# Kernel optimization log

Measured on AMD Instinct MI355X. Metric: run time of the kernel, lower is better.

The kernel has to match this reference:

```python
import jax, jax.numpy as jnp
import numpy as np

EPS = 1e-4  # Moller-Trumbore epsilon from the original

def _dot(a, b):
    return jnp.sum(a * b, axis=-1)

def setup_inputs() -> dict:
    key = jax.random.key(0)
    k1, k2, k3 = jax.random.split(key, 3)
    N, V, F = 2048, 2500, 4096
    p = jax.random.normal(k1, (N, 3), dtype=jnp.float32)
    v = jax.random.normal(k2, (V, 3), dtype=jnp.float32)
    f = jax.random.randint(k3, (F, 3), 0, V, dtype=jnp.int64)
    return {"p": p, "v": v, "f": f}

def reference(p, v, f):
    N = p.shape[0]
    faces = v[f]                      # (F,3,3)
    a, b, c = faces[:, 0], faces[:, 1], faces[:, 2]   # (F,3) each
    pe = p[None]                      # (1,N,3), broadcasts against (F,1,3)

    # --- point-to-triangle distance = min over the 3 edge segments (matches original output math) ---
    e1 = a - b                        # faces[:,0]-faces[:,1]
    e2 = c - b
    e3 = c - a

    def seg(e, ref_pt, q0, q1):
        # s = ((ref_pt - p) . e) / |e|^2, clamped; closest = s*q0 + (1-s)*q1  (original formula kept verbatim)
        m2 = _dot(e, e)[:, None]                       # (F,1)
        s = jnp.clip(_dot(ref_pt[:, None] - pe, e[:, None]) / m2, 0.0, 1.0)[..., None]  # (F,N,1)
        cl = s * q0[:, None] + (1.0 - s) * q1[:, None]  # (F,N,3)
        d = jnp.linalg.norm(cl - pe, axis=-1)           # (F,N)
        return d, cl

    d12, c12 = seg(e1, a, b, a)   # s12 from (p0-p).e1; closest = s*p1+(1-s)*p0
    d23, c23 = seg(e2, c, b, c)   # s23 from (p2-p).e2; closest = s*p1+(1-s)*p2
    d31, c31 = seg(e3, c, a, c)   # s31 from (p2-p).e3; closest = s*p0+(1-s)*p2

    d_all = jnp.stack([d12, d23, d31], axis=0)          # (3,F,N)
    c_all = jnp.stack([c12, c23, c31], axis=0)          # (3,F,N,3)
    which = jnp.argmin(d_all, axis=0)                   # (F,N)
    dist = jnp.min(d_all, axis=0)                       # (F,N)
    closest = jnp.take_along_axis(c_all, which[None, ..., None], axis=0)[0]  # (F,N,3)

    # nearest face per query point
    fidx = jnp.argmin(jnp.abs(dist), axis=0)            # (N,)
    dmin = jnp.take_along_axis(dist, fidx[None], axis=0)  # (1,N)
    closest_p = closest[fidx, jnp.arange(N)]            # (N,3)

    # --- Moller-Trumbore ray-triangle parity test toward mesh centroid ---
    dirv = v.mean(axis=0)[None] - p                     # (N,3)
    me1 = b - a                                         # faces[:,1]-faces[:,0]
    me2 = c - a
    pvec = jnp.cross(dirv[None], me2[:, None])          # (F,N,3)
    det = _dot(me1[:, None], pvec)                      # (F,N)
    tvec = pe - a[:, None]                              # (F,N,3)
    u = _dot(tvec, pvec) / det
    qvec = jnp.cross(tvec, me1[:, None])                # (F,N,3)
    dd = _dot(dirv[None], qvec) / det
    t = _dot(me2[:, None], qvec) / det
    hit = (jnp.abs(det) > EPS) & (u >= 0) & (u <= 1) & (dd >= 0) & (u + dd <= 1) & (t > EPS)
    counts = jnp.sum(hit, axis=0)                       # (N,)
    inside = (0.5 - (counts % 2 == 1).astype(dmin.dtype)) * 2.0  # +1 outside, -1 inside

    dmin = dmin * inside[None]                          # (1,N)
    return (dmin, closest_p)
```

## Files before the change

kernel.cpp:

```cpp
#include <hip/hip_runtime.h>
#include <math.h>

#define TRI_EPS 1e-4f

__global__ __launch_bounds__(256) void prep_kernel(
    const float* __restrict__ v, const int* __restrict__ f,
    float4* __restrict__ fdat6, float4* __restrict__ fdat5,
    float* __restrict__ vm, int V, int F) {
    const int t = threadIdx.x;
    const int j = blockIdx.x * 256 + t;
    if (j < F) {
        const int i0 = f[3 * j + 0];
        const int i1 = f[3 * j + 1];
        const int i2 = f[3 * j + 2];
        const float ax = v[3 * i0 + 0], ay = v[3 * i0 + 1], az = v[3 * i0 + 2];
        const float bx = v[3 * i1 + 0], by = v[3 * i1 + 1], bz = v[3 * i1 + 2];
        const float cx = v[3 * i2 + 0], cy = v[3 * i2 + 1], cz = v[3 * i2 + 2];
        const float e1x = ax - bx, e1y = ay - by, e1z = az - bz;
        const float e2x = cx - bx, e2y = cy - by, e2z = cz - bz;
        const float e3x = cx - ax, e3y = cy - ay, e3z = cz - az;
        const float m1 = e1x * e1x + e1y * e1y + e1z * e1z;
        const float m2 = e2x * e2x + e2y * e2y + e2z * e2z;
        const float m3 = e3x * e3x + e3y * e3y + e3z * e3z;
        const float inv1 = 1.f / m1, inv2 = 1.f / m2, inv3 = 1.f / m3;
        fdat6[6 * j + 0] = make_float4(ax, ay, az, inv1);
        fdat6[6 * j + 1] = make_float4(bx, by, bz, inv2);
        fdat6[6 * j + 2] = make_float4(cx, cy, cz, inv3);
        fdat6[6 * j + 3] = make_float4(e1x, e1y, e1z, 0.f);
        fdat6[6 * j + 4] = make_float4(e2x, e2y, e2z, 0.f);
        fdat6[6 * j + 5] = make_float4(e3x, e3y, e3z, 0.f);
        fdat5[5 * j + 0] = make_float4(ax, ay, az, inv1);
        fdat5[5 * j + 1] = make_float4(cx, cy, cz, inv2);
        fdat5[5 * j + 2] = make_float4(e1x, e1y, e1z, inv3);
        fdat5[5 * j + 3] = make_float4(e2x, e2y, e2z, 0.f);
        fdat5[5 * j + 4] = make_float4(e3x, e3y, e3z, 0.f);
    }
    if (blockIdx.x == 0) {
        __shared__ float sx[256], sy[256], sz[256];
        float x = 0.f, y = 0.f, z = 0.f;
        for (int i = t; i < V; i += 256) {
            x += v[3 * i + 0];
            y += v[3 * i + 1];
            z += v[3 * i + 2];
        }
        sx[t] = x; sy[t] = y; sz[t] = z;
        __syncthreads();
        for (int off = 128; off > 0; off >>= 1) {
            if (t < off) {
                sx[t] += sx[t + off];
                sy[t] += sy[t + off];
                sz[t] += sz[t + off];
            }
            __syncthreads();
        }
        if (t == 0) {
            vm[0] = sx[0] / (float)V;
            vm[1] = sy[0] / (float)V;
            vm[2] = sz[0] / (float)V;
        }
    }
}

struct FP {
    float d1, d2, d3;
    float x1, y1, z1, x2, y2, z2, x3, y3, z3;
    float apx, apy, apz;
};

__device__ __forceinline__ FP face_point(
    const float4 ra, const float4 rb, const float4 rc,
    const float e1x, const float e1y, const float e1z,
    const float e2x, const float e2y, const float e2z,
    const float e3x, const float e3y, const float e3z,
    const float px, const float py, const float pz) {
    FP r;
    const float ax = ra.x, ay = ra.y, az = ra.z;
    const float bx = rb.x, by = rb.y, bz = rb.z;
    const float cx = rc.x, cy = rc.y, cz = rc.z;
    r.apx = ax - px; r.apy = ay - py; r.apz = az - pz;
    const float cpx = cx - px, cpy = cy - py, cpz = cz - pz;

    float s1 = (r.apx * e1x + r.apy * e1y + r.apz * e1z) * ra.w;
    s1 = fminf(fmaxf(s1, 0.f), 1.f);
    const float o1 = 1.f - s1;
    r.x1 = s1 * bx + o1 * ax;
    r.y1 = s1 * by + o1 * ay;
    r.z1 = s1 * bz + o1 * az;
    float ux = r.x1 - px, uy = r.y1 - py, uz = r.z1 - pz;
    r.d1 = ux * ux + uy * uy + uz * uz;

    float s2 = (cpx * e2x + cpy * e2y + cpz * e2z) * rb.w;
    s2 = fminf(fmaxf(s2, 0.f), 1.f);
    const float o2 = 1.f - s2;
    r.x2 = s2 * bx + o2 * cx;
    r.y2 = s2 * by + o2 * cy;
    r.z2 = s2 * bz + o2 * cz;
    ux = r.x2 - px; uy = r.y2 - py; uz = r.z2 - pz;
    r.d2 = ux * ux + uy * uy + uz * uz;

    float s3 = (cpx * e3x + cpy * e3y + cpz * e3z) * rc.w;
    s3 = fminf(fmaxf(s3, 0.f), 1.f);
    const float o3 = 1.f - s3;
    r.x3 = s3 * ax + o3 * cx;
    r.y3 = s3 * ay + o3 * cy;
    r.z3 = s3 * az + o3 * cz;
    ux = r.x3 - px; uy = r.y3 - py; uz = r.z3 - pz;
    r.d3 = ux * ux + uy * uy + uz * uz;
    return r;
}

__device__ __forceinline__ void pair_lean(
    const float4 r0, const float4 r1, const float4 r2,
    const float4 r3, const float4 r4,
    const float px, const float py, const float pz,
    const float dx, const float dy, const float dz, const int j,
    float& bd2, int& bid, int& hits) {
    const float apx = r0.x - px, apy = r0.y - py, apz = r0.z - pz;
    const float cpx = r1.x - px, cpy = r1.y - py, cpz = r1.z - pz;
    const float e1x = r2.x, e1y = r2.y, e1z = r2.z;
    const float e2x = r3.x, e2y = r3.y, e2z = r3.z;
    const float e3x = r4.x, e3y = r4.y, e3z = r4.z;

    float s1 = (apx * e1x + apy * e1y + apz * e1z) * r0.w;
    s1 = fminf(fmaxf(s1, 0.f), 1.f);
    const float u1x = apx - s1 * e1x;
    const float u1y = apy - s1 * e1y;
    const float u1z = apz - s1 * e1z;
    const float d1 = u1x * u1x + u1y * u1y + u1z * u1z;

    float s2 = (cpx * e2x + cpy * e2y + cpz * e2z) * r1.w;
    s2 = fminf(fmaxf(s2, 0.f), 1.f);
    const float u2x = cpx - s2 * e2x;
    const float u2y = cpy - s2 * e2y;
    const float u2z = cpz - s2 * e2z;
    const float d2 = u2x * u2x + u2y * u2y + u2z * u2z;

    float s3 = (cpx * e3x + cpy * e3y + cpz * e3z) * r2.w;
    s3 = fminf(fmaxf(s3, 0.f), 1.f);
    const float u3x = cpx - s3 * e3x;
    const float u3y = cpy - s3 * e3y;
    const float u3z = cpz - s3 * e3z;
    const float d3 = u3x * u3x + u3y * u3y + u3z * u3z;

    float fd2 = d1; int eid = 0;
    if (d2 < fd2) { fd2 = d2; eid = 1; }
    if (d3 < fd2) { fd2 = d3; eid = 2; }
    if (fd2 < bd2) { bd2 = fd2; bid = (j << 2) | eid; }

    const float pvx = dy * e3z - dz * e3y;
    const float pvy = dz * e3x - dx * e3z;
    const float pvz = dx * e3y - dy * e3x;
    const float det = -(e1x * pvx + e1y * pvy + e1z * pvz);
    const float tu = -(apx * pvx + apy * pvy + apz * pvz);
    const float qvx = apy * e1z - apz * e1y;
    const float qvy = apz * e1x - apx * e1z;
    const float qvz = apx * e1y - apy * e1x;
    const float td = dx * qvx + dy * qvy + dz * qvz;
    const float tn = e3x * qvx + e3y * qvy + e3z * qvz;
    const float adet = fabsf(det);
    const float sd = (det > 0.f) ? 1.f : -1.f;
    const float su = tu * sd;
    const float sq = td * sd;
    const float st = tn * sd;
    if (adet > TRI_EPS && su >= 0.f && su <= adet && sq >= 0.f &&
        (su + sq) <= adet && st > TRI_EPS * adet)
        hits++;
}

template <int CS>
__global__ __launch_bounds__(256) void sdf_main_t(
    const float* __restrict__ p, const float4* __restrict__ fd5,
    const float* __restrict__ vm,
    unsigned long long* __restrict__ keysP, unsigned* __restrict__ hitsP,
    int N, int C) {
    __shared__ float4 sfd[5 * CS];
    const int t = threadIdx.x;
    const int k = blockIdx.x % C;
    const int pg = blockIdx.x / C;
    const int j0 = k * CS;

    if (t < 5 * CS) sfd[t] = fd5[5 * j0 + t];

    const int i = pg * 256 + t;
    const bool vld = (i < N);
    const int li = vld ? i : 0;
    const float px = p[3 * li + 0];
    const float py = p[3 * li + 1];
    const float pz = p[3 * li + 2];
    const float dx = vm[0] - px;
    const float dy = vm[1] - py;
    const float dz = vm[2] - pz;

    float bd2 = INFINITY; int bid = 0x7fffffff; int hits = 0;

    __syncthreads();

    #pragma unroll 4
    for (int jj = 0; jj < CS; ++jj) {
        pair_lean(sfd[5 * jj + 0], sfd[5 * jj + 1], sfd[5 * jj + 2],
                  sfd[5 * jj + 3], sfd[5 * jj + 4],
                  px, py, pz, dx, dy, dz, j0 + jj, bd2, bid, hits);
    }

    if (vld) {
        const unsigned long long key =
            ((unsigned long long)__float_as_uint(bd2) << 32) | (unsigned int)bid;
        keysP[(size_t)k * N + i] = key;
        hitsP[(size_t)k * N + i] = (unsigned)hits;
    }
}

__global__ __launch_bounds__(256) void sdf_main_g(
    const float* __restrict__ p, const float4* __restrict__ fd5,
    const float* __restrict__ vm,
    unsigned long long* __restrict__ keysP, unsigned* __restrict__ hitsP,
    int N, int F, int C, int CS) {
    const int k = blockIdx.x % C;
    const int pg = blockIdx.x / C;
    const int i = pg * 256 + threadIdx.x;
    if (i >= N) return;
    const float px = p[3 * i + 0];
    const float py = p[3 * i + 1];
    const float pz = p[3 * i + 2];
    const float dx = vm[0] - px;
    const float dy = vm[1] - py;
    const float dz = vm[2] - pz;
    float bd2 = INFINITY; int bid = 0x7fffffff; int hits = 0;
    const int j0 = k * CS;
    const int j1 = min(F, j0 + CS);
    for (int j = j0; j < j1; ++j) {
        pair_lean(fd5[5 * j + 0], fd5[5 * j + 1], fd5[5 * j + 2],
                  fd5[5 * j + 3], fd5[5 * j + 4],
                  px, py, pz, dx, dy, dz, j, bd2, bid, hits);
    }
    const unsigned long long key =
        ((unsigned long long)__float_as_uint(bd2) << 32) | (unsigned int)bid;
    keysP[(size_t)k * N + i] = key;
    hitsP[(size_t)k * N + i] = (unsigned)hits;
}

__global__ __launch_bounds__(256) void sdf_reduce_epi(
    const float* __restrict__ p, const float4* __restrict__ fd6,
    const unsigned long long* __restrict__ keysP,
    const unsigned* __restrict__ hitsP,
    float* __restrict__ out, int N, int C) {
    const int t = threadIdx.x;
    const int q = t & 63;
    const int w = t >> 6;
    const int i = blockIdx.x * 64 + q;

    unsigned long long bk = 0xFFFFFFFFFFFFFFFFull;
    unsigned hs = 0;
    if (i < N) {
        const int kpw = C >> 2;
        int k = w * kpw;
        #pragma unroll 4
        for (int kk = 0; kk < kpw; ++kk, ++k) {
            const unsigned long long kv = keysP[(size_t)k * N + i];
            if (kv < bk) bk = kv;
            hs += hitsP[(size_t)k * N + i];
        }
    }
    __shared__ unsigned long long sk[4][64];
    __shared__ unsigned sh[4][64];
    sk[w][q] = bk;
    sh[w][q] = hs;
    __syncthreads();
    if (w == 0 && i < N) {
        #pragma unroll
        for (int ww = 1; ww < 4; ++ww) {
            const unsigned long long kv = sk[ww][q];
            if (kv < bk) bk = kv;
            hs += sh[ww][q];
        }
        const float bd2 = __uint_as_float((unsigned int)(bk >> 32));
        const int bid = (int)(unsigned int)(bk & 0xFFFFFFFFull);
        const int jw = bid >> 2;
        const int eid = bid & 3;
        const float px = p[3 * i + 0];
        const float py = p[3 * i + 1];
        const float pz = p[3 * i + 2];
        const float4 wa  = fd6[6 * jw + 0];
        const float4 wb  = fd6[6 * jw + 1];
        const float4 wc  = fd6[6 * jw + 2];
        const float4 we1 = fd6[6 * jw + 3];
        const float4 we2 = fd6[6 * jw + 4];
        const float4 we3 = fd6[6 * jw + 5];
        const FP r = face_point(wa, wb, wc, we1.x, we1.y, we1.z,
                                we2.x, we2.y, we2.z, we3.x, we3.y, we3.z,
                                px, py, pz);
        float clx = r.x1, cly = r.y1, clz = r.z1;
        if (eid == 1) { clx = r.x2; cly = r.y2; clz = r.z2; }
        if (eid == 2) { clx = r.x3; cly = r.y3; clz = r.z3; }
        const float d = sqrtf(bd2);
        out[i] = (hs & 1u) ? -d : d;
        out[N + 3 * i + 0] = clx;
        out[N + 3 * i + 1] = cly;
        out[N + 3 * i + 2] = clz;
    }
}

extern "C" void kernel_launch(void* const* d_in, const int* in_sizes, int n_in,
                              void* d_out, int out_size, void* d_ws,
                              size_t ws_size, hipStream_t stream) {
    const float* p = (const float*)d_in[0];
    const float* v = (const float*)d_in[1];
    const int* f = (const int*)d_in[2];
    float* out = (float*)d_out;

    const int N = in_sizes[0] / 3;
    const int V = in_sizes[1] / 3;
    const int F = in_sizes[2] / 3;

    const int C = 256;

    char* base = (char*)d_ws;
    float* vm = (float*)base;
    unsigned long long* keysP = (unsigned long long*)(base + 16);
    unsigned* hitsP = (unsigned*)(base + 16 + 8ull * C * N);
    size_t off = 16 + 12ull * C * N;
    off = (off + 15) & ~15ull;
    float4* fdat6 = (float4*)(base + off);
    float4* fdat5 = (float4*)(base + off + 6ull * F * sizeof(float4));

    prep_kernel<<<(F + 255) / 256, 256, 0, stream>>>(v, f, fdat6, fdat5, vm,
                                                     V, F);

    const int npg = (N + 255) / 256;
    if (F == C * 16) {
        sdf_main_t<16><<<npg * C, 256, 0, stream>>>(p, fdat5, vm, keysP, hitsP,
                                                    N, C);
    } else {
        const int CS = (F + C - 1) / C;
        sdf_main_g<<<npg * C, 256, 0, stream>>>(p, fdat5, vm, keysP, hitsP,
                                                N, F, C, CS);
    }
    sdf_reduce_epi<<<(N + 63) / 64, 256, 0, stream>>>(p, fdat6, keysP, hitsP,
                                                      out, N, C);
}
```

Before: 44.18 us.

## Process two query points per thread and split faces into more chunks

```diff
diff --git a/kernel.cpp b/kernel.cpp
--- a/kernel.cpp
+++ b/kernel.cpp
@@ -168,7 +168,7 @@
 }
 
 template <int CS>
-__global__ __launch_bounds__(256) void sdf_main_t(
+__global__ __launch_bounds__(256) void sdf_main2_t(
     const float* __restrict__ p, const float4* __restrict__ fd5,
     const float* __restrict__ vm,
     unsigned long long* __restrict__ keysP, unsigned* __restrict__ hitsP,
@@ -181,32 +181,46 @@
 
     if (t < 5 * CS) sfd[t] = fd5[5 * j0 + t];
 
-    const int i = pg * 256 + t;
-    const bool vld = (i < N);
-    const int li = vld ? i : 0;
-    const float px = p[3 * li + 0];
-    const float py = p[3 * li + 1];
-    const float pz = p[3 * li + 2];
-    const float dx = vm[0] - px;
-    const float dy = vm[1] - py;
-    const float dz = vm[2] - pz;
-
-    float bd2 = INFINITY; int bid = 0x7fffffff; int hits = 0;
+    const int iA = pg * 512 + t;
+    const int iB = iA + 256;
+    const bool vA = (iA < N);
+    const bool vB = (iB < N);
+    const int lA = vA ? iA : 0;
+    const int lB = vB ? iB : 0;
+    const float pAx = p[3 * lA + 0], pAy = p[3 * lA + 1], pAz = p[3 * lA + 2];
+    const float pBx = p[3 * lB + 0], pBy = p[3 * lB + 1], pBz = p[3 * lB + 2];
+    const float vmx = vm[0], vmy = vm[1], vmz = vm[2];
+    const float dAx = vmx - pAx, dAy = vmy - pAy, dAz = vmz - pAz;
+    const float dBx = vmx - pBx, dBy = vmy - pBy, dBz = vmz - pBz;
+
+    float Ad2 = INFINITY; int Aid = 0x7fffffff; int Ah = 0;
+    float Bd2 = INFINITY; int Bid = 0x7fffffff; int Bh = 0;
 
     __syncthreads();
 
-    #pragma unroll 4
+    #pragma unroll 2
     for (int jj = 0; jj < CS; ++jj) {
-        pair_lean(sfd[5 * jj + 0], sfd[5 * jj + 1], sfd[5 * jj + 2],
-                  sfd[5 * jj + 3], sfd[5 * jj + 4],
-                  px, py, pz, dx, dy, dz, j0 + jj, bd2, bid, hits);
-    }
-
-    if (vld) {
-        const unsigned long long key =
-            ((unsigned long long)__float_as_uint(bd2) << 32) | (unsigned int)bid;
-        keysP[(size_t)k * N + i] = key;
-        hitsP[(size_t)k * N + i] = (unsigned)hits;
+        const float4 r0 = sfd[5 * jj + 0];
+        const float4 r1 = sfd[5 * jj + 1];
+        const float4 r2 = sfd[5 * jj + 2];
+        const float4 r3 = sfd[5 * jj + 3];
+        const float4 r4 = sfd[5 * jj + 4];
+        const int j = j0 + jj;
+        pair_lean(r0, r1, r2, r3, r4, pAx, pAy, pAz, dAx, dAy, dAz, j,
+                  Ad2, Aid, Ah);
+        pair_lean(r0, r1, r2, r3, r4, pBx, pBy, pBz, dBx, dBy, dBz, j,
+                  Bd2, Bid, Bh);
+    }
+
+    if (vA) {
+        keysP[(size_t)k * N + iA] =
+            ((unsigned long long)__float_as_uint(Ad2) << 32) | (unsigned int)Aid;
+        hitsP[(size_t)k * N + iA] = (unsigned)Ah;
+    }
+    if (vB) {
+        keysP[(size_t)k * N + iB] =
+            ((unsigned long long)__float_as_uint(Bd2) << 32) | (unsigned int)Bid;
+        hitsP[(size_t)k * N + iB] = (unsigned)Bh;
     }
 }
 
@@ -233,9 +247,8 @@
                   fd5[5 * j + 3], fd5[5 * j + 4],
                   px, py, pz, dx, dy, dz, j, bd2, bid, hits);
     }
-    const unsigned long long key =
+    keysP[(size_t)k * N + i] =
         ((unsigned long long)__float_as_uint(bd2) << 32) | (unsigned int)bid;
-    keysP[(size_t)k * N + i] = key;
     hitsP[(size_t)k * N + i] = (unsigned)hits;
 }
 
@@ -312,7 +325,8 @@
     const int V = in_sizes[1] / 3;
     const int F = in_sizes[2] / 3;
 
-    const int C = 256;
+    const int C = 512;
+    const int CS = 8;
 
     char* base = (char*)d_ws;
     float* vm = (float*)base;
@@ -326,14 +340,15 @@
     prep_kernel<<<(F + 255) / 256, 256, 0, stream>>>(v, f, fdat6, fdat5, vm,
                                                      V, F);
 
-    const int npg = (N + 255) / 256;
-    if (F == C * 16) {
-        sdf_main_t<16><<<npg * C, 256, 0, stream>>>(p, fdat5, vm, keysP, hitsP,
-                                                    N, C);
+    if (F == C * CS) {
+        const int npg = (N + 511) / 512;
+        sdf_main2_t<CS><<<npg * C, 256, 0, stream>>>(p, fdat5, vm, keysP,
+                                                     hitsP, N, C);
     } else {
-        const int CS = (F + C - 1) / C;
+        const int CSg = (F + C - 1) / C;
+        const int npg = (N + 255) / 256;
         sdf_main_g<<<npg * C, 256, 0, stream>>>(p, fdat5, vm, keysP, hitsP,
-                                                N, F, C, CS);
+                                                N, F, C, CSg);
     }
     sdf_reduce_epi<<<(N + 63) / 64, 256, 0, stream>>>(p, fdat6, keysP, hitsP,
                                                       out, N, C);
```

After: 53.23 us. +20.5%, slower.

## Transpose main kernel to thread-per-face with swizzle reductions over 16-face groups

Applied to the files above, without the earlier changes.

```diff
diff --git a/kernel.cpp b/kernel.cpp
--- a/kernel.cpp
+++ b/kernel.cpp
@@ -167,46 +167,120 @@
         hits++;
 }
 
-template <int CS>
-__global__ __launch_bounds__(256) void sdf_main_t(
+#define SWZF(x, imm) \
+    __int_as_float(__builtin_amdgcn_ds_swizzle(__float_as_int(x), imm))
+
+template <int PC>
+__global__ __launch_bounds__(256, 8) void sdf_tr(
     const float* __restrict__ p, const float4* __restrict__ fd5,
     const float* __restrict__ vm,
     unsigned long long* __restrict__ keysP, unsigned* __restrict__ hitsP,
-    int N, int C) {
-    __shared__ float4 sfd[5 * CS];
+    int N, int FB) {
     const int t = threadIdx.x;
-    const int k = blockIdx.x % C;
-    const int pg = blockIdx.x / C;
-    const int j0 = k * CS;
-
-    if (t < 5 * CS) sfd[t] = fd5[5 * j0 + t];
-
-    const int i = pg * 256 + t;
-    const bool vld = (i < N);
-    const int li = vld ? i : 0;
-    const float px = p[3 * li + 0];
-    const float py = p[3 * li + 1];
-    const float pz = p[3 * li + 2];
-    const float dx = vm[0] - px;
-    const float dy = vm[1] - py;
-    const float dz = vm[2] - pz;
-
-    float bd2 = INFINITY; int bid = 0x7fffffff; int hits = 0;
-
+    const int b = blockIdx.x;
+    const int fb = b % FB;
+    const int pc = b / FB;
+    const int j = fb * 256 + t;
+
+    const float4 r0 = fd5[5 * j + 0];
+    const float4 r1 = fd5[5 * j + 1];
+    const float4 r2 = fd5[5 * j + 2];
+    const float4 r3 = fd5[5 * j + 3];
+    const float4 r4 = fd5[5 * j + 4];
+    const float ax = r0.x, ay = r0.y, az = r0.z, inv1 = r0.w;
+    const float cx = r1.x, cy = r1.y, cz = r1.z, inv2 = r1.w;
+    const float e1x = r2.x, e1y = r2.y, e1z = r2.z, inv3 = r2.w;
+    const float e2x = r3.x, e2y = r3.y, e2z = r3.z;
+    const float e3x = r4.x, e3y = r4.y, e3z = r4.z;
+
+    const float vmx = vm[0], vmy = vm[1], vmz = vm[2];
+
+    __shared__ float4 spt[PC];
+    if (t < 4 * PC) {
+        const int idx = t >> 2, c = t & 3;
+        const int gi = pc * PC + idx;
+        float val = 0.f;
+        if (c < 3 && gi < N) val = p[3 * gi + c];
+        ((float*)spt)[t] = val;
+    }
     __syncthreads();
 
-    #pragma unroll 4
-    for (int jj = 0; jj < CS; ++jj) {
-        pair_lean(sfd[5 * jj + 0], sfd[5 * jj + 1], sfd[5 * jj + 2],
-                  sfd[5 * jj + 3], sfd[5 * jj + 4],
-                  px, py, pz, dx, dy, dz, j0 + jj, bd2, bid, hits);
-    }
-
-    if (vld) {
-        const unsigned long long key =
-            ((unsigned long long)__float_as_uint(bd2) << 32) | (unsigned int)bid;
-        keysP[(size_t)k * N + i] = key;
-        hitsP[(size_t)k * N + i] = (unsigned)hits;
+    const int bid_base = (j << 2);
+    const int sh = t & 48;
+
+    for (int it = 0; it < PC; ++it) {
+        const int pt = pc * PC + it;
+        const float4 P = spt[it];
+        const float px = P.x, py = P.y, pz = P.z;
+        const float dx = vmx - px, dy = vmy - py, dz = vmz - pz;
+
+        const float apx = ax - px, apy = ay - py, apz = az - pz;
+        const float cpx = cx - px, cpy = cy - py, cpz = cz - pz;
+
+        float s1 = (apx * e1x + apy * e1y + apz * e1z) * inv1;
+        s1 = fminf(fmaxf(s1, 0.f), 1.f);
+        const float u1x = apx - s1 * e1x;
+        const float u1y = apy - s1 * e1y;
+        const float u1z = apz - s1 * e1z;
+        const float d1 = u1x * u1x + u1y * u1y + u1z * u1z;
+
+        float s2 = (cpx * e2x + cpy * e2y + cpz * e2z) * inv2;
+        s2 = fminf(fmaxf(s2, 0.f), 1.f);
+        const float u2x = cpx - s2 * e2x;
+        const float u2y = cpy - s2 * e2y;
+        const float u2z = cpz - s2 * e2z;
+        const float d2 = u2x * u2x + u2y * u2y + u2z * u2z;
+
+        float s3 = (cpx * e3x + cpy * e3y + cpz * e3z) * inv3;
+        s3 = fminf(fmaxf(s3, 0.f), 1.f);
+        const float u3x = cpx - s3 * e3x;
+        const float u3y = cpy - s3 * e3y;
+        const float u3z = cpz - s3 * e3z;
+        const float d3 = u3x * u3x + u3y * u3y + u3z * u3z;
+
+        float fd2 = d1; int eid = 0;
+        if (d2 < fd2) { fd2 = d2; eid = 1; }
+        if (d3 < fd2) { fd2 = d3; eid = 2; }
+
+        const float pvx = dy * e3z - dz * e3y;
+        const float pvy = dz * e3x - dx * e3z;
+        const float pvz = dx * e3y - dy * e3x;
+        const float det = -(e1x * pvx + e1y * pvy + e1z * pvz);
+        const float tu = -(apx * pvx + apy * pvy + apz * pvz);
+        const float qvx = apy * e1z - apz * e1y;
+        const float qvy = apz * e1x - apx * e1z;
+        const float qvz = apx * e1y - apy * e1x;
+        const float td = dx * qvx + dy * qvy + dz * qvz;
+        const float tn = e3x * qvx + e3y * qvy + e3z * qvz;
+        const float adet = fabsf(det);
+        const float sd = (det > 0.f) ? 1.f : -1.f;
+        const float su = tu * sd;
+        const float sq = td * sd;
+        const float st = tn * sd;
+        const int hit = (adet > TRI_EPS && su >= 0.f && su <= adet &&
+                         sq >= 0.f && (su + sq) <= adet &&
+                         st > TRI_EPS * adet) ? 1 : 0;
+
+        float dmin = fd2;
+        dmin = fminf(dmin, SWZF(dmin, 0x041F));
+        dmin = fminf(dmin, SWZF(dmin, 0x081F));
+        dmin = fminf(dmin, SWZF(dmin, 0x101F));
+        dmin = fminf(dmin, SWZF(dmin, 0x201F));
+        int idv = (fd2 == dmin) ? (bid_base | eid) : 0x7fffffff;
+        idv = min(idv, __builtin_amdgcn_ds_swizzle(idv, 0x041F));
+        idv = min(idv, __builtin_amdgcn_ds_swizzle(idv, 0x081F));
+        idv = min(idv, __builtin_amdgcn_ds_swizzle(idv, 0x101F));
+        idv = min(idv, __builtin_amdgcn_ds_swizzle(idv, 0x201F));
+        const unsigned long long bal = __ballot(hit);
+        const unsigned hcount = (unsigned)__popcll((bal >> sh) & 0xFFFFull);
+
+        if (((t & 15) == 0) && pt < N) {
+            const int g = (j >> 4);
+            keysP[(size_t)g * N + pt] =
+                ((unsigned long long)__float_as_uint(dmin) << 32) |
+                (unsigned int)idv;
+            hitsP[(size_t)g * N + pt] = hcount;
+        }
     }
 }
 
@@ -233,9 +307,8 @@
                   fd5[5 * j + 3], fd5[5 * j + 4],
                   px, py, pz, dx, dy, dz, j, bd2, bid, hits);
     }
-    const unsigned long long key =
+    keysP[(size_t)k * N + i] =
         ((unsigned long long)__float_as_uint(bd2) << 32) | (unsigned int)bid;
-    keysP[(size_t)k * N + i] = key;
     hitsP[(size_t)k * N + i] = (unsigned)hits;
 }
 
@@ -312,8 +385,7 @@
     const int V = in_sizes[1] / 3;
     const int F = in_sizes[2] / 3;
 
-    const int C = 256;
-
+    const int C = (F % 256 == 0) ? (F / 16) : 256;
     char* base = (char*)d_ws;
     float* vm = (float*)base;
     unsigned long long* keysP = (unsigned long long*)(base + 16);
@@ -326,12 +398,15 @@
     prep_kernel<<<(F + 255) / 256, 256, 0, stream>>>(v, f, fdat6, fdat5, vm,
                                                      V, F);
 
-    const int npg = (N + 255) / 256;
-    if (F == C * 16) {
-        sdf_main_t<16><<<npg * C, 256, 0, stream>>>(p, fdat5, vm, keysP, hitsP,
-                                                    N, C);
+    if (F % 256 == 0) {
+        const int FB = F / 256;
+        const int PC = 16;
+        const int npc = (N + PC - 1) / PC;
+        sdf_tr<16><<<FB * npc, 256, 0, stream>>>(p, fdat5, vm, keysP, hitsP,
+                                                 N, FB);
     } else {
         const int CS = (F + C - 1) / C;
+        const int npg = (N + 255) / 256;
         sdf_main_g<<<npg * C, 256, 0, stream>>>(p, fdat5, vm, keysP, hitsP,
                                                 N, F, C, CS);
     }
```

Result: slower. 47.16 us (+6.8%).
